# Kernel optimization log

Hardware: AMD Instinct MI355X
Metric: run time of the kernel (lower is better)

Reference implementation:

```python
import jax, jax.numpy as jnp
import numpy as np

D_MODEL = 1024
D_STATE = 128
D_CONV = 4
EXPAND = 2
HEADDIM = 64
D_INNER = EXPAND * D_MODEL          # 2048
NHEADS = D_INNER // HEADDIM          # 32
CONV_CH = D_INNER + 2 * D_STATE      # conv acts on x, B, C (ngroups=1)
D_IN_PROJ = 2 * D_INNER + 2 * D_STATE + NHEADS
CHUNK = 128


def setup_inputs() -> dict:
    key = jax.random.key(0)
    ks = jax.random.split(key, 8)
    B, L = 4, 2048
    return {
        'x': jax.random.normal(ks[0], (B, L, D_MODEL), jnp.float32),
        'ln_w': jnp.ones((D_MODEL,), jnp.float32),
        'ln_b': jnp.zeros((D_MODEL,), jnp.float32),
        'in_proj_w': jax.random.normal(ks[1], (D_IN_PROJ, D_MODEL), jnp.float32) * 0.02,
        'conv_w': jax.random.normal(ks[2], (CONV_CH, D_CONV), jnp.float32) * 0.2,
        'conv_b': jnp.zeros((CONV_CH,), jnp.float32),
        'dt_bias': jax.random.normal(ks[3], (NHEADS,), jnp.float32) * 0.5,
        'A_log': jax.random.uniform(ks[4], (NHEADS,), jnp.float32, 0.0, 1.5),
        'D': jax.random.normal(ks[5], (NHEADS,), jnp.float32) * 0.1 + 1.0,
        'norm_w': jnp.ones((D_INNER,), jnp.float32),
        'out_proj_w': jax.random.normal(ks[6], (D_MODEL, D_INNER), jnp.float32) * 0.02,
    }


def segsum(a):
    # a: (..., T) -> (..., T, T) with out[i, j] = sum_{j < k <= i} a[k], -inf above diag
    T = a.shape[-1]
    a_rep = jnp.broadcast_to(a[..., :, None], a.shape + (T,))
    a_masked = jnp.where(jnp.tril(jnp.ones((T, T), bool), -1), a_rep, 0.0)
    seg = jnp.cumsum(a_masked, axis=-2)
    return jnp.where(jnp.tril(jnp.ones((T, T), bool), 0), seg, -jnp.inf)


def _ssd(X, a, Bm, Cm):
    # Chunked SSD (Mamba2). X: (b,l,h,p) pre-multiplied by dt; a: (b,l,h)=dt*A; Bm,Cm: (b,l,n)
    b, l, h, p = X.shape
    c = l // CHUNK
    Xc = X.reshape(b, c, CHUNK, h, p)
    Bc = Bm.reshape(b, c, CHUNK, -1)
    Cc = Cm.reshape(b, c, CHUNK, -1)
    ac = a.reshape(b, c, CHUNK, h).transpose(0, 3, 1, 2)   # (b,h,c,q)
    a_cs = jnp.cumsum(ac, axis=-1)                          # (b,h,c,q)
    Lm = jnp.exp(segsum(ac))                                # (b,h,c,q,q)
    # intra-chunk (diagonal) part
    Y_diag = jnp.einsum('bcln,bcsn,bhcls,bcshp->bclhp', Cc, Bc, Lm, Xc)
    # chunk final states
    decay_states = jnp.exp(a_cs[..., -1:] - a_cs)           # (b,h,c,q)
    states = jnp.einsum('bcln,bhcl,bclhp->bchpn', Bc, decay_states, Xc)
    states = jnp.concatenate([jnp.zeros_like(states[:, :1]), states], axis=1)  # (b,c+1,h,p,n)
    a_chunk = jnp.pad(a_cs[..., -1], ((0, 0), (0, 0), (1, 0)))  # (b,h,c+1)
    decay_chunk = jnp.exp(segsum(a_chunk))                  # (b,h,c+1,c+1)
    prev_states = jnp.einsum('bhzc,bchpn->bzhpn', decay_chunk, states)[:, :-1]  # (b,c,h,p,n)
    # inter-chunk (off-diagonal) part
    Y_off = jnp.einsum('bcln,bchpn,bhcl->bclhp', Cc, prev_states, jnp.exp(a_cs))
    return (Y_diag + Y_off).reshape(b, l, h, p)


def reference(x, ln_w, ln_b, in_proj_w, conv_w, conv_b, dt_bias, A_log, D, norm_w, out_proj_w):
    B, L, _ = x.shape
    # pre-LayerNorm
    mu = x.mean(-1, keepdims=True)
    var = ((x - mu) ** 2).mean(-1, keepdims=True)
    h = (x - mu) / jnp.sqrt(var + 1e-5) * ln_w + ln_b
    # Mamba2 in_proj -> [z, xBC, dt]
    zxbcdt = h @ in_proj_w.T
    z = zxbcdt[..., :D_INNER]
    xBC = zxbcdt[..., D_INNER:D_INNER + CONV_CH]
    dt = jax.nn.softplus(zxbcdt[..., -NHEADS:] + dt_bias)  # (B,L,H)
    # causal depthwise conv1d + SiLU
    xp = jnp.pad(xBC, ((0, 0), (D_CONV - 1, 0), (0, 0)))
    conv = sum(xp[:, k:k + L, :] * conv_w[:, k] for k in range(D_CONV)) + conv_b
    xBC = jax.nn.silu(conv)
    xs = xBC[..., :D_INNER].reshape(B, L, NHEADS, HEADDIM)
    Bm = xBC[..., D_INNER:D_INNER + D_STATE]
    Cm = xBC[..., D_INNER + D_STATE:]
    A = -jnp.exp(A_log)                                    # (H,)
    Y = _ssd(xs * dt[..., None], dt * A, Bm, Cm)
    Y = Y + D[None, None, :, None] * xs                    # D skip connection
    y = Y.reshape(B, L, D_INNER)
    # gated RMSNorm (norm_before_gate=False)
    y = y * jax.nn.silu(z)
    y = y * jax.lax.rsqrt(jnp.mean(y * y, -1, keepdims=True) + 1e-5) * norm_w
    out = y @ out_proj_w.T
    # dropout in eval mode = identity; residual
    return out + x
```

## Files before the change

### kernel.cpp

```cpp
#include <hip/hip_runtime.h>
#include <math.h>

#define BATCH   4
#define LSEQ    2048
#define DMODEL  1024
#define DSTATE  128
#define HEADDIM 64
#define DINNER  2048
#define NHEADS  32
#define CONVCH  2304
#define DINPROJ 4384
#define NPAD    4480
#define CHUNKL  128
#define NCHUNK  16
#define ROWS    (BATCH*LSEQ)

#define B_Z     ((size_t)0)
#define B_XBC   (B_Z   + (size_t)ROWS*DINNER*2)
#define B_DT    (B_XBC + (size_t)ROWS*CONVCH*2)
#define B_XS    (B_DT  + (size_t)ROWS*NHEADS*4)
#define B_BC    (B_XS  + (size_t)ROWS*DINNER*2)
#define B_Y     (B_BC  + (size_t)ROWS*256*2)
#define B_ASUM  (B_Y   + (size_t)ROWS*DINNER*2)
#define B_END   (B_ASUM + (size_t)BATCH*NCHUNK*NHEADS*4)

typedef __attribute__((ext_vector_type(8))) short bf16x8;
typedef __attribute__((ext_vector_type(4))) float f32x4;

__device__ __forceinline__ float b2f(ushort u) {
  union { uint32_t i; float f; } v; v.i = ((uint32_t)u) << 16; return v.f;
}
__device__ __forceinline__ ushort f2b(float f) {
  union { float f; uint32_t i; } v; v.f = f;
  uint32_t r = (v.i + 0x7FFFu + ((v.i >> 16) & 1u)) >> 16;
  return (ushort)r;
}

__device__ __forceinline__ void async_ld16(const void* g, void* l) {
  __builtin_amdgcn_global_load_lds(
      (const __attribute__((address_space(1))) unsigned int*)g,
      (__attribute__((address_space(3))) unsigned int*)l, 16, 0, 0);
}

template<int K>
__device__ __forceinline__ void gemm_core_swz(const ushort* __restrict__ A,
    const ushort* __restrict__ W, int m0, int n0, int tid,
    ushort* lA, ushort* lB, f32x4 acc[4][4])
{
  const int lane = tid & 63;
  const int w = tid >> 6;
  const int wm = (w & 1) * 64;
  const int wn = (w >> 1) * 64;
  const int rl = lane & 15;
  const int q  = lane >> 4;
  for (int k0 = 0; k0 < K; k0 += 64) {
    __syncthreads();
    #pragma unroll
    for (int is = 0; is < 4; is++) {
      int s = (w*4 + is)*64 + lane;
      int row = s >> 3;
      int g = (s & 7) ^ (row & 7);
      async_ld16(A + (size_t)(m0 + row)*K + k0 + g*8, lA + (size_t)s*8);
      async_ld16(W + (size_t)(n0 + row)*K + k0 + g*8, lB + (size_t)s*8);
    }
    __syncthreads();
    #pragma unroll
    for (int kh = 0; kh < 2; kh++) {
      bf16x8 af[4], bfr[4];
      #pragma unroll
      for (int i = 0; i < 4; i++) {
        int row = wm + i*16 + rl;
        af[i] = *(const bf16x8*)&lA[(size_t)(row*8 + ((kh*4 + q) ^ (row & 7)))*8];
      }
      #pragma unroll
      for (int j = 0; j < 4; j++) {
        int row = wn + j*16 + rl;
        bfr[j] = *(const bf16x8*)&lB[(size_t)(row*8 + ((kh*4 + q) ^ (row & 7)))*8];
      }
      #pragma unroll
      for (int i = 0; i < 4; i++)
        #pragma unroll
        for (int j = 0; j < 4; j++)
          acc[i][j] = __builtin_amdgcn_mfma_f32_16x16x32_bf16(af[i], bfr[j], acc[i][j], 0, 0, 0);
    }
  }
}

__global__ __launch_bounds__(256) void convert_win_kernel(const float* __restrict__ W,
                                                          ushort* __restrict__ Wb)
{
  size_t i = (size_t)blockIdx.x*256 + threadIdx.x;
  Wb[i] = (i < (size_t)DINPROJ*DMODEL) ? f2b(W[i]) : (ushort)0;
}

__global__ __launch_bounds__(256) void convert_wout_kernel(const float* __restrict__ W,
                                                           ushort* __restrict__ Wb)
{
  size_t i = (size_t)blockIdx.x*256 + threadIdx.x;
  Wb[i] = f2b(W[i]);
}

__global__ __launch_bounds__(256) void ln_kernel(const float* __restrict__ x,
    const float* __restrict__ w, const float* __restrict__ bias, ushort* __restrict__ h)
{
  const int row = blockIdx.x;
  const int t = threadIdx.x;
  const float* xr = x + (size_t)row * DMODEL;
  float v[4];
  float s = 0.f;
  #pragma unroll
  for (int i = 0; i < 4; i++) { v[i] = xr[t + i*256]; s += v[i]; }
  __shared__ float red[4];
  #pragma unroll
  for (int o = 32; o > 0; o >>= 1) s += __shfl_down(s, o, 64);
  if ((t & 63) == 0) red[t >> 6] = s;
  __syncthreads();
  float mean = (red[0]+red[1]+red[2]+red[3]) * (1.f/DMODEL);
  float vs = 0.f;
  #pragma unroll
  for (int i = 0; i < 4; i++) { float d = v[i]-mean; vs += d*d; }
  #pragma unroll
  for (int o = 32; o > 0; o >>= 1) vs += __shfl_down(vs, o, 64);
  __syncthreads();
  if ((t & 63) == 0) red[t >> 6] = vs;
  __syncthreads();
  float rstd = rsqrtf((red[0]+red[1]+red[2]+red[3]) * (1.f/DMODEL) + 1e-5f);
  ushort* hr = h + (size_t)row * DMODEL;
  #pragma unroll
  for (int i = 0; i < 4; i++) {
    int c = t + i*256;
    hr[c] = f2b((v[i]-mean)*rstd*w[c] + bias[c]);
  }
}

__global__ __launch_bounds__(256) void gemm_inproj_mfma(const ushort* __restrict__ A,
    const ushort* __restrict__ W, ushort* __restrict__ z, ushort* __restrict__ xbc,
    float* __restrict__ dtr, const float* __restrict__ dtb)
{
  __shared__ ushort smem[128*136];
  ushort* lA = smem;
  ushort* lB = smem + 8192;
  const int tid = threadIdx.x;
  const int lane = tid & 63;
  const int w = tid >> 6;
  const int m0 = blockIdx.x * 128;
  const int n0 = blockIdx.y * 128;
  const int wm = (w & 1) * 64;
  const int wn = (w >> 1) * 64;
  f32x4 acc[4][4];
  #pragma unroll
  for (int i = 0; i < 4; i++)
    #pragma unroll
    for (int j = 0; j < 4; j++) acc[i][j] = (f32x4)(0.f);

  gemm_core_swz<DMODEL>(A, W, m0, n0, tid, lA, lB, acc);

  const int col_l = lane & 15;
  const int row_l = (lane >> 4) * 4;
  __syncthreads();
  if (n0 < DINNER + CONVCH) {
    #pragma unroll
    for (int i = 0; i < 4; i++)
      #pragma unroll
      for (int j = 0; j < 4; j++)
        #pragma unroll
        for (int r = 0; r < 4; r++)
          smem[(wm + i*16 + row_l + r)*136 + wn + j*16 + col_l] = f2b(acc[i][j][r]);
    __syncthreads();
    ushort* outp; int coff, ncols;
    if (n0 < DINNER) { outp = z;   coff = n0;          ncols = DINNER; }
    else             { outp = xbc; coff = n0 - DINNER; ncols = CONVCH; }
    #pragma unroll
    for (int it = 0; it < 8; it++) {
      int idx = tid + it*256;
      int row = idx >> 4, c8 = idx & 15;
      *(uint4*)(outp + (size_t)(m0 + row)*ncols + coff + c8*8) = *(const uint4*)&smem[row*136 + c8*8];
    }
  } else {
    #pragma unroll
    for (int i = 0; i < 4; i++)
      #pragma unroll
      for (int j = 0; j < 2; j++) {
        int lc = wn + j*16 + col_l;
        if (lc < 32) {
          float bb = dtb[lc];
          #pragma unroll
          for (int r = 0; r < 4; r++) {
            float v = acc[i][j][r] + bb;
            v = (v > 20.f) ? v : log1pf(expf(v));
            dtr[(size_t)(m0 + wm + i*16 + row_l + r)*NHEADS + lc] = v;
          }
        }
      }
  }
}

__global__ __launch_bounds__(256) void gemm_outproj_mfma(const ushort* __restrict__ A,
    const ushort* __restrict__ W, const float* __restrict__ x, float* __restrict__ out)
{
  __shared__ ushort smem[17408];
  ushort* lA = smem;
  ushort* lB = smem + 8192;
  float* fbuf = (float*)smem;
  const int tid = threadIdx.x;
  const int lane = tid & 63;
  const int w = tid >> 6;
  const int m0 = blockIdx.x * 128;
  const int n0 = blockIdx.y * 128;
  const int wn = (w >> 1) * 64;
  f32x4 acc[4][4];
  #pragma unroll
  for (int i = 0; i < 4; i++)
    #pragma unroll
    for (int j = 0; j < 4; j++) acc[i][j] = (f32x4)(0.f);

  gemm_core_swz<DINNER>(A, W, m0, n0, tid, lA, lB, acc);

  const int colL = lane & 15;
  const int rowQ = (lane >> 4) * 4;
  #pragma unroll
  for (int h0 = 0; h0 < 2; h0++) {
    __syncthreads();
    if ((w & 1) == h0) {
      #pragma unroll
      for (int i = 0; i < 4; i++)
        #pragma unroll
        for (int j = 0; j < 4; j++)
          #pragma unroll
          for (int r = 0; r < 4; r++)
            fbuf[(i*16 + rowQ + r)*132 + wn + j*16 + colL] = acc[i][j][r];
    }
    __syncthreads();
    #pragma unroll
    for (int it = 0; it < 8; it++) {
      int idx = tid + it*256;
      int row = idx >> 5, c4 = idx & 31;
      int gm = m0 + h0*64 + row;
      float4 xv = *(const float4*)(x + (size_t)gm*DMODEL + n0 + c4*4);
      float4 vv = *(const float4*)&fbuf[row*132 + c4*4];
      vv.x += xv.x; vv.y += xv.y; vv.z += xv.z; vv.w += xv.w;
      *(float4*)(out + (size_t)gm*DMODEL + n0 + c4*4) = vv;
    }
  }
}

__global__ __launch_bounds__(256) void conv_tiled(const ushort* __restrict__ xbc,
    const float* __restrict__ cw, const float* __restrict__ cb,
    ushort* __restrict__ xs, ushort* __restrict__ bcb)
{
  __shared__ ushort tile[35*256];
  const int tid = threadIdx.x;
  const int ch0 = blockIdx.x * 256;
  const int row0 = blockIdx.y * 32;
  const int l0 = row0 & (LSEQ-1);
  for (int idx = tid; idx < 35*32; idx += 256) {
    int r = idx >> 5, c16 = idx & 31;
    uint4 v = make_uint4(0,0,0,0);
    if (l0 + r - 3 >= 0)
      v = *(const uint4*)(xbc + (size_t)(row0 + r - 3)*CONVCH + ch0 + c16*8);
    *(uint4*)&tile[r*256 + c16*8] = v;
  }
  __syncthreads();
  const int ch = ch0 + tid;
  const float w0 = cw[ch*4+0], w1 = cw[ch*4+1], w2 = cw[ch*4+2], w3 = cw[ch*4+3];
  const float bias = cb[ch];
  const bool isX = (ch0 < DINNER);
  #pragma unroll 4
  for (int r = 0; r < 32; r++) {
    float acc = bias;
    acc = fmaf(b2f(tile[(r+0)*256 + tid]), w0, acc);
    acc = fmaf(b2f(tile[(r+1)*256 + tid]), w1, acc);
    acc = fmaf(b2f(tile[(r+2)*256 + tid]), w2, acc);
    acc = fmaf(b2f(tile[(r+3)*256 + tid]), w3, acc);
    float v = acc / (1.f + expf(-acc));
    if (isX) xs[(size_t)(row0 + r)*DINNER + ch] = f2b(v);
    else     bcb[(size_t)(row0 + r)*256 + (ch - DINNER)] = f2b(v);
  }
}

__global__ __launch_bounds__(256) void states_mfma(
    const ushort* __restrict__ xs, const ushort* __restrict__ bcb, const float* __restrict__ dt,
    const float* __restrict__ A_log, ushort* __restrict__ S, float* __restrict__ asum)
{
  constexpr int LDP = 136;
  __shared__ ushort lBT[128*LDP];
  __shared__ ushort lXT[64*LDP];
  __shared__ float dts[CHUNKL], acs[CHUNKL];
  __shared__ float wtot;
  const int hh = blockIdx.x, c = blockIdx.y, b = blockIdx.z;
  const int tid = threadIdx.x;
  const int lane = tid & 63;
  const int w = tid >> 6;
  const int rbase = b*LSEQ + c*CHUNKL;
  const size_t sbase = (size_t)((b*NCHUNK + c)*NHEADS + hh) * 8192;

  float pre = 0.f;
  if (tid < 128) {
    float myv = dt[(size_t)(rbase + tid)*NHEADS + hh];
    dts[tid] = myv;
    pre = myv;
    #pragma unroll
    for (int o = 1; o < 64; o <<= 1) {
      float u = __shfl_up(pre, o, 64);
      if ((tid & 63) >= o) pre += u;
    }
    if (tid == 63) wtot = pre;
  }
  #pragma unroll
  for (int it = 0; it < 8; it++) {
    int chunk = tid + it*256;
    int l = chunk >> 4, n8 = chunk & 15;
    ushort tmp[8];
    *(uint4*)tmp = *(const uint4*)(bcb + (size_t)(rbase + l)*256 + n8*8);
    #pragma unroll
    for (int u = 0; u < 8; u++) lBT[(n8*8+u)*LDP + l] = tmp[u];
  }
  __syncthreads();
  float alast_loc = 0.f;
  if (tid < 128) {
    float Aval = -expf(A_log[hh]);
    float a = (pre + ((tid >= 64) ? wtot : 0.f)) * Aval;
    acs[tid] = a;
    if (tid == 127) { asum[(b*NCHUNK + c)*NHEADS + hh] = a; }
  }
  __syncthreads();
  alast_loc = acs[CHUNKL-1];
  #pragma unroll
  for (int it = 0; it < 4; it++) {
    int chunk = tid + it*256;
    int l = chunk >> 3, p8 = (chunk & 7)*8;
    ushort tmp[8];
    *(uint4*)tmp = *(const uint4*)(xs + (size_t)(rbase + l)*DINNER + hh*HEADDIM + p8);
    float wl = dts[l] * expf(alast_loc - acs[l]);
    #pragma unroll
    for (int u = 0; u < 8; u++) lXT[(p8+u)*LDP + l] = f2b(b2f(tmp[u]) * wl);
  }
  __syncthreads();

  const int rl = lane & 15;
  const int kq = (lane >> 4) * 8;
  const int nb = w * 32;
  f32x4 acc[4][2];
  #pragma unroll
  for (int i = 0; i < 4; i++) { acc[i][0] = (f32x4)(0.f); acc[i][1] = (f32x4)(0.f); }
  #pragma unroll
  for (int k0 = 0; k0 < 128; k0 += 32) {
    bf16x8 af[4], bfr[2];
    #pragma unroll
    for (int i = 0; i < 4; i++) af[i]  = *(const bf16x8*)&lXT[(i*16 + rl)*LDP + k0 + kq];
    #pragma unroll
    for (int j = 0; j < 2; j++) bfr[j] = *(const bf16x8*)&lBT[(nb + j*16 + rl)*LDP + k0 + kq];
    #pragma unroll
    for (int i = 0; i < 4; i++)
      #pragma unroll
      for (int j = 0; j < 2; j++)
        acc[i][j] = __builtin_amdgcn_mfma_f32_16x16x32_bf16(af[i], bfr[j], acc[i][j], 0, 0, 0);
  }
  __syncthreads();
  const int colL = lane & 15;
  const int rowQ = (lane >> 4) * 4;
  #pragma unroll
  for (int i = 0; i < 4; i++)
    #pragma unroll
    for (int j = 0; j < 2; j++)
      #pragma unroll
      for (int r = 0; r < 4; r++)
        lXT[(i*16 + rowQ + r)*LDP + nb + j*16 + colL] = f2b(acc[i][j][r]);
  __syncthreads();
  #pragma unroll
  for (int it = 0; it < 4; it++) {
    int idx = tid + it*256;
    int row = idx >> 4, c8 = idx & 15;
    *(uint4*)(S + sbase + row*128 + c8*8) = *(const uint4*)&lXT[row*LDP + c8*8];
  }
}

__global__ __launch_bounds__(256) void scan_kernel(ushort* __restrict__ S, const float* __restrict__ asum)
{
  const int hh = blockIdx.x, sl = blockIdx.y, b = blockIdx.z;
  const int base0 = sl*2048 + threadIdx.x;
  float carry[8];
  #pragma unroll
  for (int i = 0; i < 8; i++) carry[i] = 0.f;
  for (int c = 0; c < NCHUNK; c++) {
    ushort* Sp = S + (size_t)((b*NCHUNK + c)*NHEADS + hh) * 8192;
    float dec = expf(asum[(b*NCHUNK + c)*NHEADS + hh]);
    #pragma unroll
    for (int i = 0; i < 8; i++) {
      int idx = base0 + i*256;
      float sv = b2f(Sp[idx]);
      Sp[idx] = f2b(carry[i]);
      carry[i] = fmaf(dec, carry[i], sv);
    }
  }
}

__global__ __launch_bounds__(256) void yssd_mfma(
    const ushort* __restrict__ xs, const ushort* __restrict__ bcb, const float* __restrict__ dt,
    const float* __restrict__ A_log, const float* __restrict__ Dvec,
    const ushort* __restrict__ S, ushort* __restrict__ y)
{
  constexpr int LDP = 136;
  __shared__ ushort lC [128*LDP];
  __shared__ ushort lBM[128*LDP];
  __shared__ ushort lP [64*LDP];
  __shared__ ushort lXT[64*LDP];
  __shared__ float dts[CHUNKL], acs[CHUNKL];
  __shared__ float wtot;
  const int hh = blockIdx.x, c = blockIdx.y, b = blockIdx.z;
  const int tid = threadIdx.x;
  const int lane = tid & 63;
  const int w = tid >> 6;
  const int rbase = b*LSEQ + c*CHUNKL;
  const size_t sbase = (size_t)((b*NCHUNK + c)*NHEADS + hh) * 8192;

  #pragma unroll
  for (int it = 0; it < 8; it++) {
    int chunk = tid + it*256;
    int l = chunk >> 4, c8 = chunk & 15;
    const ushort* src = bcb + (size_t)(rbase + l)*256 + c8*8;
    *(uint4*)&lBM[l*LDP + c8*8] = *(const uint4*)src;
    *(uint4*)&lC [l*LDP + c8*8] = *(const uint4*)(src + 128);
  }
  #pragma unroll
  for (int it = 0; it < 4; it++) {
    int chunk = tid + it*256;
    int p = chunk >> 4, c8 = chunk & 15;
    *(uint4*)&lP[p*LDP + c8*8] = *(const uint4*)(S + sbase + p*128 + c8*8);
  }
  #pragma unroll
  for (int it = 0; it < 4; it++) {
    int chunk = tid + it*256;
    int s = chunk >> 3, p0 = (chunk & 7)*8;
    ushort tmp[8];
    *(uint4*)tmp = *(const uint4*)(xs + (size_t)(rbase + s)*DINNER + hh*HEADDIM + p0);
    #pragma unroll
    for (int u = 0; u < 8; u++) lXT[(p0+u)*LDP + s] = tmp[u];
  }
  float pre = 0.f;
  if (tid < 128) {
    float myv = dt[(size_t)(rbase + tid)*NHEADS + hh];
    dts[tid] = myv;
    pre = myv;
    #pragma unroll
    for (int o = 1; o < 64; o <<= 1) {
      float u = __shfl_up(pre, o, 64);
      if ((tid & 63) >= o) pre += u;
    }
    if (tid == 63) wtot = pre;
  }
  __syncthreads();
  if (tid < 128) {
    float Aval = -expf(A_log[hh]);
    acs[tid] = (pre + ((tid >= 64) ? wtot : 0.f)) * Aval;
  }

  const int rl = lane & 15;
  const int kq = (lane >> 4) * 8;
  const int colL = lane & 15;
  const int rowQ = (lane >> 4) * 4;

  const int wm = (w & 1) * 64;
  const int wn = (w >> 1) * 64;
  f32x4 G[4][4];
  #pragma unroll
  for (int i = 0; i < 4; i++)
    #pragma unroll
    for (int j = 0; j < 4; j++) G[i][j] = (f32x4)(0.f);
  #pragma unroll
  for (int k0 = 0; k0 < 128; k0 += 32) {
    bf16x8 af[4], bfr[4];
    #pragma unroll
    for (int i = 0; i < 4; i++) af[i]  = *(const bf16x8*)&lC [(wm + i*16 + rl)*LDP + k0 + kq];
    #pragma unroll
    for (int j = 0; j < 4; j++) bfr[j] = *(const bf16x8*)&lBM[(wn + j*16 + rl)*LDP + k0 + kq];
    #pragma unroll
    for (int i = 0; i < 4; i++)
      #pragma unroll
      for (int j = 0; j < 4; j++)
        G[i][j] = __builtin_amdgcn_mfma_f32_16x16x32_bf16(af[i], bfr[j], G[i][j], 0, 0, 0);
  }
  __syncthreads();

  #pragma unroll
  for (int j = 0; j < 4; j++) {
    int sIdx = wn + j*16 + colL;
    float as = acs[sIdx];
    float ds = dts[sIdx];
    #pragma unroll
    for (int i = 0; i < 4; i++) {
      #pragma unroll
      for (int r = 0; r < 4; r++) {
        int lIdx = wm + i*16 + rowQ + r;
        float m = (lIdx >= sIdx) ? G[i][j][r] * expf(acs[lIdx] - as) * ds : 0.f;
        lBM[lIdx*LDP + sIdx] = f2b(m);
      }
    }
  }

  const int om = w * 32;
  f32x4 Y[2][4];
  #pragma unroll
  for (int i = 0; i < 2; i++)
    #pragma unroll
    for (int j = 0; j < 4; j++) Y[i][j] = (f32x4)(0.f);
  #pragma unroll
  for (int k0 = 0; k0 < 128; k0 += 32) {
    bf16x8 a2[2], b2[4];
    #pragma unroll
    for (int i = 0; i < 2; i++) a2[i] = *(const bf16x8*)&lC[(om + i*16 + rl)*LDP + k0 + kq];
    #pragma unroll
    for (int j = 0; j < 4; j++) b2[j] = *(const bf16x8*)&lP[(j*16 + rl)*LDP + k0 + kq];
    #pragma unroll
    for (int i = 0; i < 2; i++)
      #pragma unroll
      for (int j = 0; j < 4; j++)
        Y[i][j] = __builtin_amdgcn_mfma_f32_16x16x32_bf16(a2[i], b2[j], Y[i][j], 0, 0, 0);
  }
  #pragma unroll
  for (int i = 0; i < 2; i++)
    #pragma unroll
    for (int r = 0; r < 4; r++) {
      float e = expf(acs[om + i*16 + rowQ + r]);
      #pragma unroll
      for (int j = 0; j < 4; j++) Y[i][j][r] *= e;
    }
  __syncthreads();

  #pragma unroll
  for (int k0 = 0; k0 < 128; k0 += 32) {
    bf16x8 a3[2], b3[4];
    #pragma unroll
    for (int i = 0; i < 2; i++) a3[i] = *(const bf16x8*)&lBM[(om + i*16 + rl)*LDP + k0 + kq];
    #pragma unroll
    for (int j = 0; j < 4; j++) b3[j] = *(const bf16x8*)&lXT[(j*16 + rl)*LDP + k0 + kq];
    #pragma unroll
    for (int i = 0; i < 2; i++)
      #pragma unroll
      for (int j = 0; j < 4; j++)
        Y[i][j] = __builtin_amdgcn_mfma_f32_16x16x32_bf16(a3[i], b3[j], Y[i][j], 0, 0, 0);
  }

  const float Dh = Dvec[hh];
  #pragma unroll
  for (int i = 0; i < 2; i++) {
    #pragma unroll
    for (int r = 0; r < 4; r++) {
      int lIdx = om + i*16 + rowQ + r;
      ushort* yrow = y + (size_t)(rbase + lIdx)*DINNER + hh*HEADDIM;
      #pragma unroll
      for (int j = 0; j < 4; j++) {
        int p = j*16 + colL;
        float val = Y[i][j][r] + Dh * b2f(lXT[p*LDP + lIdx]);
        yrow[p] = f2b(val);
      }
    }
  }
}

__global__ __launch_bounds__(256) void rmsnorm_kernel(ushort* __restrict__ y,
    const ushort* __restrict__ z, const float* __restrict__ nw)
{
  const int row = blockIdx.x;
  const int t = threadIdx.x;
  ushort* yr = y + (size_t)row*DINNER;
  const ushort* zr = z + (size_t)row*DINNER;
  float v[8];
  float ss = 0.f;
  #pragma unroll
  for (int i = 0; i < 8; i++) {
    int c = t + i*256;
    float zz = b2f(zr[c]);
    float g = b2f(yr[c]) * (zz / (1.f + expf(-zz)));
    v[i] = g;
    ss += g*g;
  }
  #pragma unroll
  for (int o = 32; o > 0; o >>= 1) ss += __shfl_down(ss, o, 64);
  __shared__ float red[4];
  if ((t & 63) == 0) red[t >> 6] = ss;
  __syncthreads();
  float scale = rsqrtf((red[0]+red[1]+red[2]+red[3]) * (1.f/DINNER) + 1e-5f);
  #pragma unroll
  for (int i = 0; i < 8; i++) {
    int c = t + i*256;
    yr[c] = f2b(v[i]*scale*nw[c]);
  }
}

extern "C" void kernel_launch(void* const* d_in, const int* in_sizes, int n_in,
                              void* d_out, int out_size, void* d_ws, size_t ws_size,
                              hipStream_t stream)
{
  const float* x    = (const float*)d_in[0];
  const float* lnw  = (const float*)d_in[1];
  const float* lnb  = (const float*)d_in[2];
  const float* win  = (const float*)d_in[3];
  const float* cw   = (const float*)d_in[4];
  const float* cb   = (const float*)d_in[5];
  const float* dtb  = (const float*)d_in[6];
  const float* alog = (const float*)d_in[7];
  const float* dvec = (const float*)d_in[8];
  const float* nw   = (const float*)d_in[9];
  const float* wout = (const float*)d_in[10];
  float* out = (float*)d_out;
  char* ws = (char*)d_ws;
  (void)in_sizes; (void)n_in; (void)out_size;

  if (ws_size < B_END) return;

  ushort* zb   = (ushort*)(ws + B_Z);
  ushort* xbcb = (ushort*)(ws + B_XBC);
  float*  dtr  = (float*) (ws + B_DT);
  ushort* xsb  = (ushort*)(ws + B_XS);
  ushort* bcb  = (ushort*)(ws + B_BC);
  ushort* yb   = (ushort*)(ws + B_Y);
  float*  asum = (float*) (ws + B_ASUM);
  ushort* Sb   = xbcb;
  ushort* hb   = yb;
  ushort* winB = (ushort*)(ws + B_Y + (size_t)ROWS*DMODEL*2);
  ushort* woutB= (ushort*)(ws + B_XBC + (size_t)BATCH*NCHUNK*NHEADS*HEADDIM*DSTATE*2);

  hipLaunchKernelGGL(convert_win_kernel, dim3((NPAD*DMODEL)/256), dim3(256), 0, stream, win, winB);
  hipLaunchKernelGGL(ln_kernel, dim3(ROWS), dim3(256), 0, stream, x, lnw, lnb, hb);
  hipLaunchKernelGGL(gemm_inproj_mfma, dim3(64, 35), dim3(256), 0, stream, hb, winB, zb, xbcb, dtr, dtb);
  hipLaunchKernelGGL(conv_tiled, dim3(9, ROWS/32), dim3(256), 0, stream, xbcb, cw, cb, xsb, bcb);
  hipLaunchKernelGGL(convert_wout_kernel, dim3((DMODEL*DINNER)/256), dim3(256), 0, stream, wout, woutB);
  hipLaunchKernelGGL(states_mfma, dim3(NHEADS, NCHUNK, BATCH), dim3(256), 0, stream,
                     xsb, bcb, dtr, alog, Sb, asum);
  hipLaunchKernelGGL(scan_kernel, dim3(NHEADS, 4, BATCH), dim3(256), 0, stream, Sb, asum);
  hipLaunchKernelGGL(yssd_mfma, dim3(NHEADS, NCHUNK, BATCH), dim3(256), 0, stream,
                     xsb, bcb, dtr, alog, dvec, Sb, yb);
  hipLaunchKernelGGL(rmsnorm_kernel, dim3(ROWS), dim3(256), 0, stream, yb, zb, nw);
  hipLaunchKernelGGL(gemm_outproj_mfma, dim3(64, 8), dim3(256), 0, stream, yb, woutB, x, out);
}
```

Measured before the change: 480.5 us.

## Read SSD operands directly from global and swizzle GEMM epilogue LDS

The yssd kernel stops staging B, C and the chunk-state matrix into shared memory and loads MFMA fragments straight from global memory. This cuts its LDS footprint from roughly 100KB to about 52KB, allowing more blocks per CU, and removes the staging pass. The two GEMM epilogues replace padded LDS rows with an XOR swizzle so the staging buffer fits within the operand tiles (16384 elements), also saving LDS. The cost is repeated uncoalesced global/L2 reads of C, B and the state in the SSD kernel.

```diff
diff --git a/kernel.cpp b/kernel.cpp
--- a/kernel.cpp
+++ b/kernel.cpp
@@ -137,7 +137,7 @@
     const ushort* __restrict__ W, ushort* __restrict__ z, ushort* __restrict__ xbc,
     float* __restrict__ dtr, const float* __restrict__ dtb)
 {
-  __shared__ ushort smem[128*136];
+  __shared__ ushort smem[16384];
   ushort* lA = smem;
   ushort* lB = smem + 8192;
   const int tid = threadIdx.x;
@@ -162,10 +162,15 @@
     #pragma unroll
     for (int i = 0; i < 4; i++)
       #pragma unroll
-      for (int j = 0; j < 4; j++)
+      for (int j = 0; j < 4; j++) {
+        int col = wn + j*16 + col_l;
+        int g = col >> 3;
         #pragma unroll
-        for (int r = 0; r < 4; r++)
-          smem[(wm + i*16 + row_l + r)*136 + wn + j*16 + col_l] = f2b(acc[i][j][r]);
+        for (int r = 0; r < 4; r++) {
+          int row = wm + i*16 + row_l + r;
+          smem[row*128 + ((g ^ (row & 7)) << 3) + (col & 7)] = f2b(acc[i][j][r]);
+        }
+      }
     __syncthreads();
     ushort* outp; int coff, ncols;
     if (n0 < DINNER) { outp = z;   coff = n0;          ncols = DINNER; }
@@ -174,7 +179,8 @@
     for (int it = 0; it < 8; it++) {
       int idx = tid + it*256;
       int row = idx >> 4, c8 = idx & 15;
-      *(uint4*)(outp + (size_t)(m0 + row)*ncols + coff + c8*8) = *(const uint4*)&smem[row*136 + c8*8];
+      *(uint4*)(outp + (size_t)(m0 + row)*ncols + coff + c8*8) =
+          *(const uint4*)&smem[row*128 + ((c8 ^ (row & 7)) << 3)];
     }
   } else {
     #pragma unroll
@@ -198,7 +204,7 @@
 __global__ __launch_bounds__(256) void gemm_outproj_mfma(const ushort* __restrict__ A,
     const ushort* __restrict__ W, const float* __restrict__ x, float* __restrict__ out)
 {
-  __shared__ ushort smem[17408];
+  __shared__ ushort smem[16384];
   ushort* lA = smem;
   ushort* lB = smem + 8192;
   float* fbuf = (float*)smem;
@@ -225,10 +231,15 @@
       #pragma unroll
       for (int i = 0; i < 4; i++)
         #pragma unroll
-        for (int j = 0; j < 4; j++)
+        for (int j = 0; j < 4; j++) {
+          int col = wn + j*16 + colL;
+          int g = col >> 2;
           #pragma unroll
-          for (int r = 0; r < 4; r++)
-            fbuf[(i*16 + rowQ + r)*132 + wn + j*16 + colL] = acc[i][j][r];
+          for (int r = 0; r < 4; r++) {
+            int row = i*16 + rowQ + r;
+            fbuf[row*128 + ((g ^ (row & 7)) << 2) + (col & 3)] = acc[i][j][r];
+          }
+        }
     }
     __syncthreads();
     #pragma unroll
@@ -237,7 +248,7 @@
       int row = idx >> 5, c4 = idx & 31;
       int gm = m0 + h0*64 + row;
       float4 xv = *(const float4*)(x + (size_t)gm*DMODEL + n0 + c4*4);
-      float4 vv = *(const float4*)&fbuf[row*132 + c4*4];
+      float4 vv = *(const float4*)&fbuf[row*128 + ((c4 ^ (row & 7)) << 2)];
       vv.x += xv.x; vv.y += xv.y; vv.z += xv.z; vv.w += xv.w;
       *(float4*)(out + (size_t)gm*DMODEL + n0 + c4*4) = vv;
     }
@@ -401,9 +412,7 @@
     const ushort* __restrict__ S, ushort* __restrict__ y)
 {
   constexpr int LDP = 136;
-  __shared__ ushort lC [128*LDP];
-  __shared__ ushort lBM[128*LDP];
-  __shared__ ushort lP [64*LDP];
+  __shared__ ushort lM [128*LDP];
   __shared__ ushort lXT[64*LDP];
   __shared__ float dts[CHUNKL], acs[CHUNKL];
   __shared__ float wtot;
@@ -413,21 +422,9 @@
   const int w = tid >> 6;
   const int rbase = b*LSEQ + c*CHUNKL;
   const size_t sbase = (size_t)((b*NCHUNK + c)*NHEADS + hh) * 8192;
-
-  #pragma unroll
-  for (int it = 0; it < 8; it++) {
-    int chunk = tid + it*256;
-    int l = chunk >> 4, c8 = chunk & 15;
-    const ushort* src = bcb + (size_t)(rbase + l)*256 + c8*8;
-    *(uint4*)&lBM[l*LDP + c8*8] = *(const uint4*)src;
-    *(uint4*)&lC [l*LDP + c8*8] = *(const uint4*)(src + 128);
-  }
-  #pragma unroll
-  for (int it = 0; it < 4; it++) {
-    int chunk = tid + it*256;
-    int p = chunk >> 4, c8 = chunk & 15;
-    *(uint4*)&lP[p*LDP + c8*8] = *(const uint4*)(S + sbase + p*128 + c8*8);
-  }
+  const ushort* Bg = bcb + (size_t)rbase*256;
+  const ushort* Cg = Bg + 128;
+
   #pragma unroll
   for (int it = 0; it < 4; it++) {
     int chunk = tid + it*256;
@@ -471,9 +468,9 @@
   for (int k0 = 0; k0 < 128; k0 += 32) {
     bf16x8 af[4], bfr[4];
     #pragma unroll
-    for (int i = 0; i < 4; i++) af[i]  = *(const bf16x8*)&lC [(wm + i*16 + rl)*LDP + k0 + kq];
-    #pragma unroll
-    for (int j = 0; j < 4; j++) bfr[j] = *(const bf16x8*)&lBM[(wn + j*16 + rl)*LDP + k0 + kq];
+    for (int i = 0; i < 4; i++) af[i]  = *(const bf16x8*)(Cg + (size_t)(wm + i*16 + rl)*256 + k0 + kq);
+    #pragma unroll
+    for (int j = 0; j < 4; j++) bfr[j] = *(const bf16x8*)(Bg + (size_t)(wn + j*16 + rl)*256 + k0 + kq);
     #pragma unroll
     for (int i = 0; i < 4; i++)
       #pragma unroll
@@ -493,7 +490,7 @@
       for (int r = 0; r < 4; r++) {
         int lIdx = wm + i*16 + rowQ + r;
         float m = (lIdx >= sIdx) ? G[i][j][r] * expf(acs[lIdx] - as) * ds : 0.f;
-        lBM[lIdx*LDP + sIdx] = f2b(m);
+        lM[lIdx*LDP + sIdx] = f2b(m);
       }
     }
   }
@@ -508,9 +505,9 @@
   for (int k0 = 0; k0 < 128; k0 += 32) {
     bf16x8 a2[2], b2[4];
     #pragma unroll
-    for (int i = 0; i < 2; i++) a2[i] = *(const bf16x8*)&lC[(om + i*16 + rl)*LDP + k0 + kq];
-    #pragma unroll
-    for (int j = 0; j < 4; j++) b2[j] = *(const bf16x8*)&lP[(j*16 + rl)*LDP + k0 + kq];
+    for (int i = 0; i < 2; i++) a2[i] = *(const bf16x8*)(Cg + (size_t)(om + i*16 + rl)*256 + k0 + kq);
+    #pragma unroll
+    for (int j = 0; j < 4; j++) b2[j] = *(const bf16x8*)(S + sbase + (size_t)(j*16 + rl)*128 + k0 + kq);
     #pragma unroll
     for (int i = 0; i < 2; i++)
       #pragma unroll
@@ -531,7 +528,7 @@
   for (int k0 = 0; k0 < 128; k0 += 32) {
     bf16x8 a3[2], b3[4];
     #pragma unroll
-    for (int i = 0; i < 2; i++) a3[i] = *(const bf16x8*)&lBM[(om + i*16 + rl)*LDP + k0 + kq];
+    for (int i = 0; i < 2; i++) a3[i] = *(const bf16x8*)&lM[(om + i*16 + rl)*LDP + k0 + kq];
     #pragma unroll
     for (int j = 0; j < 4; j++) b3[j] = *(const bf16x8*)&lXT[(j*16 + rl)*LDP + k0 + kq];
     #pragma unroll
```

Result: faster. 459.6 us (-4.4%).
